# Kernel tuning notes

Hardware: AMD Instinct MI355X
Metric: run time of the kernel (lower is better)

The kernel has to match this reference:

```python
import jax, jax.numpy as jnp
import numpy as np

HEAD_DIM = 256
NUM_HEADS = 8
NUM_KV = 1
MAX_WAVELENGTH = 10000.0


def _apply_rope(x, positions):
    # x: [B, S, N, H], positions: [B, S] int
    d = x.shape[-1]
    freq_exponents = (2.0 / d) * jnp.arange(d // 2, dtype=jnp.float32)
    timescale = MAX_WAVELENGTH ** freq_exponents  # [H/2]
    radians = positions[..., None].astype(jnp.float32) / timescale  # [B, S, H/2]
    radians = radians[..., None, :]  # [B, S, 1, H/2]
    sin, cos = jnp.sin(radians), jnp.cos(radians)
    first, second = jnp.split(x.astype(jnp.float32), 2, axis=-1)
    out = jnp.concatenate([first * cos - second * sin, second * cos + first * sin], axis=-1)
    return out.astype(x.dtype)


def setup_inputs() -> dict:
    key = jax.random.key(0)
    ks = jax.random.split(key, 8)
    B, S0, S1 = 4, 768, 256
    W0, W1 = 2048, 1024
    T = S0 + S1
    s = 0.02  # param init scale
    x0 = jax.random.normal(ks[0], (B, S0, W0), jnp.float32)
    x1 = jax.random.normal(ks[1], (B, S1, W1), jnp.float32)
    w_q0 = jax.random.normal(ks[2], (NUM_HEADS, W0, HEAD_DIM), jnp.float32) * s
    w_kv0 = jax.random.normal(ks[3], (2, NUM_KV, W0, HEAD_DIM), jnp.float32) * s
    w_out0 = jax.random.normal(ks[4], (NUM_HEADS, HEAD_DIM, W0), jnp.float32) * s
    w_q1 = jax.random.normal(ks[5], (NUM_HEADS, W1, HEAD_DIM), jnp.float32) * s
    w_kv1 = jax.random.normal(ks[6], (2, NUM_KV, W1, HEAD_DIM), jnp.float32) * s
    w_out1 = jax.random.normal(ks[7], (NUM_HEADS, HEAD_DIM, W1), jnp.float32) * s
    positions = jnp.broadcast_to(jnp.arange(T, dtype=jnp.int32), (B, T))
    attn_mask = jnp.broadcast_to(jnp.tril(jnp.ones((T, T), bool))[None, None], (B, 1, T, T))
    return {"x0": x0, "x1": x1, "w_q0": w_q0, "w_kv0": w_kv0, "w_out0": w_out0,
            "w_q1": w_q1, "w_kv1": w_kv1, "w_out1": w_out1,
            "positions": positions, "attn_mask": attn_mask}


def reference(x0, x1, w_q0, w_kv0, w_out0, w_q1, w_kv1, w_out1, positions, attn_mask):
    dtype = x0.dtype
    # GQA projections per stream (num_kv_heads != num_heads path)
    q0 = jnp.einsum('BTD,NDH->BTNH', x0, w_q0)
    k0, v0 = jnp.einsum('BSD,CKDH->CBSKH', x0, w_kv0)
    q1 = jnp.einsum('BTD,NDH->BTNH', x1, w_q1)
    k1, v1 = jnp.einsum('BSD,CKDH->CBSKH', x1, w_kv1)
    q = jnp.concatenate([q0, q1], axis=1)  # [B, T, N, H]
    k = jnp.concatenate([k0, k1], axis=1)  # [B, T, K, H]
    v = jnp.concatenate([v0, v1], axis=1)
    q = _apply_rope(q, positions) * (HEAD_DIM ** -0.5)
    k = _apply_rope(k, positions)
    B, T = q.shape[0], q.shape[1]
    G = NUM_HEADS // NUM_KV
    q = q.reshape(B, T, NUM_KV, G, HEAD_DIM)
    logits = jnp.einsum('BTKGH,BSKH->BKGTS', q, k, preferred_element_type=jnp.float32)
    big_neg = -2.3819763e38
    masked = jnp.where(attn_mask[:, :, None, :, :], logits, big_neg)
    probs = jax.nn.softmax(masked, axis=-1).astype(dtype)
    encoded = jnp.einsum('BKGTS,BSKH->BTKGH', probs, v).reshape(B, T, NUM_HEADS, HEAD_DIM)
    S0 = x0.shape[1]
    out0 = jnp.einsum('BTNH,NHD->BTD', encoded[:, :S0], w_out0)
    out1 = jnp.einsum('BTNH,NHD->BTD', encoded[:, S0:], w_out1)
    return (out0, out1, k, v)
```

## Files before the change

### kernel.cpp

```cpp
#include <hip/hip_runtime.h>
#include <hip/hip_bf16.h>

typedef __attribute__((ext_vector_type(8))) short bf16x8;
typedef __attribute__((ext_vector_type(4))) float f32x4;
typedef __attribute__((ext_vector_type(4))) unsigned short u16x4;
typedef unsigned short US;

__device__ __forceinline__ f32x4 mfma16(bf16x8 a, bf16x8 b, f32x4 c) {
  return __builtin_amdgcn_mfma_f32_16x16x32_bf16(a, b, c, 0, 0, 0);
}

__device__ __forceinline__ US f2bf(float f) {
  union { float f; unsigned u; } x; x.f = f;
  unsigned r = x.u + 0x7fffu + ((x.u >> 16) & 1u);
  return (US)(r >> 16);
}

__device__ __forceinline__ void gld16(const US* gp, US* lp) {
  __builtin_amdgcn_global_load_lds(
      (const __attribute__((address_space(1))) unsigned*)gp,
      (__attribute__((address_space(3))) unsigned*)lp, 16, 0, 0);
}

__device__ __forceinline__ int map_row(int r, int mode) {
  if (mode == 1) { int b = r / 768; return b * 1024 + (r - b * 768); }
  if (mode == 2) { int b = r >> 8; return b * 1024 + 768 + (r & 255); }
  return r;
}

__global__ void k_cast(const float* __restrict__ src, US* __restrict__ dst, int n4) {
  int i = blockIdx.x * 256 + threadIdx.x;
  if (i >= n4) return;
  f32x4 v = *reinterpret_cast<const f32x4*>(src + (size_t)i * 4);
  u16x4 o;
  o[0] = f2bf(v[0]); o[1] = f2bf(v[1]); o[2] = f2bf(v[2]); o[3] = f2bf(v[3]);
  *reinterpret_cast<u16x4*>(dst + (size_t)i * 4) = o;
}

__global__ __launch_bounds__(256)
void k_tpack(const float* __restrict__ src, US* __restrict__ dst,
             int R, int C, long sbs, long dbs) {
  __shared__ float tile[32][33];
  int c0 = blockIdx.x * 32, r0 = blockIdx.y * 32;
  src += (long)blockIdx.z * sbs;
  dst += (long)blockIdx.z * dbs;
  int tx = threadIdx.x, ty = threadIdx.y;
#pragma unroll
  for (int i = 0; i < 4; ++i)
    tile[ty + 8 * i][tx] = src[(size_t)(r0 + ty + 8 * i) * C + c0 + tx];
  __syncthreads();
#pragma unroll
  for (int i = 0; i < 4; ++i)
    dst[(size_t)(c0 + ty + 8 * i) * R + r0 + tx] = f2bf(tile[tx][ty + 8 * i]);
}

template <int CMAP>
__global__ __launch_bounds__(256, 2)
void k_gemm_qkv(const US* __restrict__ A, const US* __restrict__ BT,
                float* __restrict__ Cq, float* __restrict__ Ckv,
                int M, int K) {
  __shared__ __align__(16) US lA[2][128 * 32];
  __shared__ __align__(16) US lB[2][128 * 32];
  const int tid = threadIdx.x;
  const int lane = tid & 63;
  const int wid = tid >> 6;
  const int wm = wid >> 1, wn = wid & 1;
  const int m0 = blockIdx.y * 128, n0 = blockIdx.x * 128;
  const int g = lane >> 4, c = lane & 15;
  const int lrow = lane >> 2, lcol = (lane & 3) * 8;
  const size_t ga0 = (size_t)(m0 + wid * 16 + lrow) * K + lcol;
  const size_t ga1 = (size_t)(m0 + 64 + wid * 16 + lrow) * K + lcol;
  const size_t gb0 = (size_t)(n0 + wid * 16 + lrow) * K + lcol;
  const size_t gb1 = (size_t)(n0 + 64 + wid * 16 + lrow) * K + lcol;

  auto stage = [&](int bi, int k0) {
    gld16(A + ga0 + k0, &lA[bi][(wid * 16) * 32]);
    gld16(A + ga1 + k0, &lA[bi][(64 + wid * 16) * 32]);
    gld16(BT + gb0 + k0, &lB[bi][(wid * 16) * 32]);
    gld16(BT + gb1 + k0, &lB[bi][(64 + wid * 16) * 32]);
  };

  f32x4 acc[4][4];
#pragma unroll
  for (int i = 0; i < 4; ++i)
#pragma unroll
    for (int j = 0; j < 4; ++j) acc[i][j] = f32x4{0.f, 0.f, 0.f, 0.f};

  const int nt = K >> 5;
  stage(0, 0);
  __syncthreads();
  for (int t = 0; t < nt; ++t) {
    const int bi = t & 1;
    if (t + 1 < nt) stage(bi ^ 1, (t + 1) * 32);
    bf16x8 af[4], bfr[4];
#pragma unroll
    for (int i = 0; i < 4; ++i) {
      af[i] = *reinterpret_cast<const bf16x8*>(&lA[bi][(wm * 64 + i * 16 + c) * 32 + g * 8]);
      bfr[i] = *reinterpret_cast<const bf16x8*>(&lB[bi][(wn * 64 + i * 16 + c) * 32 + g * 8]);
    }
#pragma unroll
    for (int i = 0; i < 4; ++i)
#pragma unroll
      for (int j = 0; j < 4; ++j)
        acc[i][j] = mfma16(af[i], bfr[j], acc[i][j]);
    __syncthreads();
  }

  const bool isq = (n0 < 2048);
  float* Cb = isq ? Cq : Ckv;
  const int Nst = isq ? 2048 : 512;
  const int nb = (isq ? n0 : n0 - 2048) + wn * 64 + c;
#pragma unroll
  for (int i = 0; i < 4; ++i) {
#pragma unroll
    for (int r = 0; r < 4; ++r) {
      int orow = map_row(m0 + wm * 64 + i * 16 + 4 * g + r, CMAP);
      float* cp = Cb + (size_t)orow * Nst + nb;
#pragma unroll
      for (int j = 0; j < 4; ++j) cp[j * 16] = acc[i][j][r];
    }
  }
}

__global__ __launch_bounds__(256, 2)
void k_gemm_out(const US* __restrict__ A, const US* __restrict__ BT0, const US* __restrict__ BT1,
                float* __restrict__ C0, float* __restrict__ C1) {
  const int m0 = blockIdx.y * 128, n0 = blockIdx.x * 128;
  const int s0 = m0 & 1023;
  const bool is0 = (s0 < 768);
  if (!is0 && n0 >= 1024) return;
  const US* __restrict__ BT = is0 ? BT0 : BT1;
  const int K = 2048;
  __shared__ __align__(16) US lA[2][128 * 32];
  __shared__ __align__(16) US lB[2][128 * 32];
  const int tid = threadIdx.x;
  const int lane = tid & 63;
  const int wid = tid >> 6;
  const int wm = wid >> 1, wn = wid & 1;
  const int g = lane >> 4, c = lane & 15;
  const int lrow = lane >> 2, lcol = (lane & 3) * 8;
  const size_t ga0 = (size_t)(m0 + wid * 16 + lrow) * K + lcol;
  const size_t ga1 = (size_t)(m0 + 64 + wid * 16 + lrow) * K + lcol;
  const size_t gb0 = (size_t)(n0 + wid * 16 + lrow) * K + lcol;
  const size_t gb1 = (size_t)(n0 + 64 + wid * 16 + lrow) * K + lcol;

  auto stage = [&](int bi, int k0) {
    gld16(A + ga0 + k0, &lA[bi][(wid * 16) * 32]);
    gld16(A + ga1 + k0, &lA[bi][(64 + wid * 16) * 32]);
    gld16(BT + gb0 + k0, &lB[bi][(wid * 16) * 32]);
    gld16(BT + gb1 + k0, &lB[bi][(64 + wid * 16) * 32]);
  };

  f32x4 acc[4][4];
#pragma unroll
  for (int i = 0; i < 4; ++i)
#pragma unroll
    for (int j = 0; j < 4; ++j) acc[i][j] = f32x4{0.f, 0.f, 0.f, 0.f};

  const int nt = K >> 5;
  stage(0, 0);
  __syncthreads();
  for (int t = 0; t < nt; ++t) {
    const int bi = t & 1;
    if (t + 1 < nt) stage(bi ^ 1, (t + 1) * 32);
    bf16x8 af[4], bfr[4];
#pragma unroll
    for (int i = 0; i < 4; ++i) {
      af[i] = *reinterpret_cast<const bf16x8*>(&lA[bi][(wm * 64 + i * 16 + c) * 32 + g * 8]);
      bfr[i] = *reinterpret_cast<const bf16x8*>(&lB[bi][(wn * 64 + i * 16 + c) * 32 + g * 8]);
    }
#pragma unroll
    for (int i = 0; i < 4; ++i)
#pragma unroll
      for (int j = 0; j < 4; ++j)
        acc[i][j] = mfma16(af[i], bfr[j], acc[i][j]);
    __syncthreads();
  }

  const int col = n0 + wn * 64 + c;
#pragma unroll
  for (int i = 0; i < 4; ++i) {
#pragma unroll
    for (int r = 0; r < 4; ++r) {
      const int rf = m0 + wm * 64 + i * 16 + 4 * g + r;
      const int b = rf >> 10, s = rf & 1023;
      float* cp = is0 ? (C0 + (size_t)(b * 768 + s) * 2048 + col)
                      : (C1 + (size_t)(b * 256 + s - 768) * 1024 + col);
#pragma unroll
      for (int j = 0; j < 4; ++j) cp[j * 16] = acc[i][j][r];
    }
  }
}

__global__ __launch_bounds__(256)
void k_rope(const float* __restrict__ q_raw, const float* __restrict__ kv_raw,
            const int* __restrict__ pos, US* __restrict__ q_bf,
            US* __restrict__ k_bf, float* __restrict__ k_out) {
  __shared__ float sa[128], ca[128];
  const int bt = blockIdx.x;
  const int tid = threadIdx.x;
  const int p = pos[bt];
  if (tid < 128) {
    float inv_ts = powf(10000.0f, -(float)tid * (1.0f / 128.0f));
    float r = (float)p * inv_ts;
    sa[tid] = sinf(r);
    ca[tid] = cosf(r);
  }
  __syncthreads();
  const float scale = 0.0625f;
  const size_t qo = (size_t)bt * 2048;
#pragma unroll
  for (int it = 0; it < 4; ++it) {
    int idx = it * 256 + tid;
    int n = idx >> 7, j = idx & 127;
    float x1 = q_raw[qo + n * 256 + j];
    float x2 = q_raw[qo + n * 256 + j + 128];
    float s = sa[j], co = ca[j];
    q_bf[qo + n * 256 + j] = f2bf(scale * (x1 * co - x2 * s));
    q_bf[qo + n * 256 + j + 128] = f2bf(scale * (x2 * co + x1 * s));
  }
  if (tid < 128) {
    int j = tid;
    const size_t ko = (size_t)bt * 512;
    float x1 = kv_raw[ko + j], x2 = kv_raw[ko + j + 128];
    float s = sa[j], co = ca[j];
    float o1 = x1 * co - x2 * s, o2 = x2 * co + x1 * s;
    const size_t kd = (size_t)bt * 256;
    k_bf[kd + j] = f2bf(o1);
    k_bf[kd + j + 128] = f2bf(o2);
    k_out[kd + j] = o1;
    k_out[kd + j + 128] = o2;
  }
}

__global__ __launch_bounds__(256)
void k_vtrans(const float* __restrict__ kv_raw, float* __restrict__ v_out, US* __restrict__ vt) {
  __shared__ float tile[32][33];
  int t0 = blockIdx.x * 32, h0 = blockIdx.y * 32, b = blockIdx.z;
  int tx = threadIdx.x, ty = threadIdx.y;
#pragma unroll
  for (int i = 0; i < 4; ++i) {
    int t = t0 + ty + 8 * i;
    float v = kv_raw[(size_t)(b * 1024 + t) * 512 + 256 + h0 + tx];
    tile[ty + 8 * i][tx] = v;
    v_out[(size_t)(b * 1024 + t) * 256 + h0 + tx] = v;
  }
  __syncthreads();
#pragma unroll
  for (int i = 0; i < 4; ++i) {
    int h = h0 + ty + 8 * i;
    vt[(size_t)(b * 256 + h) * 1024 + t0 + tx] = f2bf(tile[tx][ty + 8 * i]);
  }
}

__global__ __launch_bounds__(256, 2)
void k_attn(const US* __restrict__ qb, const US* __restrict__ kb,
            const US* __restrict__ vt, US* __restrict__ enc) {
  __shared__ __align__(16) US lK[2][32 * 256];
  __shared__ __align__(16) US lV[2][256 * 32];
  const int id = blockIdx.x;
  const int r0_ = (id < 256) ? id : 767 - id;
  const int qt = 63 - (r0_ >> 3);
  const int hg = (r0_ >> 2) & 1;
  const int b = r0_ & 3;
  const int tid = threadIdx.x;
  const int wid = tid >> 6;
  const int lane = tid & 63;
  const int g = lane >> 4, c = lane & 15;
  const int qbase = qt * 16;
  const int n = hg * 4 + wid;

  const US* kbB = kb + (size_t)b * 262144;
  const US* vtB = vt + (size_t)b * 262144;

  bf16x8 qf[8];
  {
    const US* qp = qb + ((size_t)((b * 1024 + qbase + c) * 8 + n)) * 256 + 8 * g;
#pragma unroll
    for (int ch = 0; ch < 8; ++ch)
      qf[ch] = *reinterpret_cast<const bf16x8*>(qp + ch * 32);
  }

  auto stage = [&](int bi, int c0) {
#pragma unroll
    for (int j = 0; j < 4; ++j) {
      const int rk = wid * 8 + j * 2 + (lane >> 5);
      const int sk = lane & 31;
      gld16(kbB + (size_t)(c0 + rk) * 256 + (sk ^ (rk & 7)) * 8,
            &lK[bi][(wid * 8 + j * 2) * 256]);
      const int rv = wid * 64 + j * 16 + (lane >> 2);
      const int sv = lane & 3;
      gld16(vtB + (size_t)rv * 1024 + c0 + (sv ^ ((rv >> 1) & 3)) * 8,
            &lV[bi][(wid * 64 + j * 16) * 32]);
    }
  };

  f32x4 acc[16];
#pragma unroll
  for (int i = 0; i < 16; ++i) acc[i] = f32x4{0.f, 0.f, 0.f, 0.f};
  float m_run = -3.0e38f, l_run = 0.f;

  const int nC = qbase / 32 + 1;
  stage(0, 0);
  __syncthreads();

  for (int i = 0; i < nC; ++i) {
    const int c0 = 32 * i;
    const int bi = i & 1;
    if (i + 1 < nC) stage(bi ^ 1, c0 + 32);

    const bool hb = (c0 + 16 <= qbase);
    f32x4 sA = {0.f, 0.f, 0.f, 0.f}, sB = {0.f, 0.f, 0.f, 0.f};
#pragma unroll
    for (int ch = 0; ch < 8; ++ch) {
      const int slot = (((ch * 4 + g) ^ (c & 7)) * 8);
      sA = mfma16(*reinterpret_cast<const bf16x8*>(&lK[bi][c * 256 + slot]), qf[ch], sA);
    }
    if (hb) {
#pragma unroll
      for (int ch = 0; ch < 8; ++ch) {
        const int slot = (((ch * 4 + g) ^ (c & 7)) * 8);
        sB = mfma16(*reinterpret_cast<const bf16x8*>(&lK[bi][(c + 16) * 256 + slot]), qf[ch], sB);
      }
    }
    if (c0 == qbase) {
#pragma unroll
      for (int r = 0; r < 4; ++r)
        if (4 * g + r > c) sA[r] = -3.0e38f;
    }
    if (hb && (c0 + 16 == qbase)) {
#pragma unroll
      for (int r = 0; r < 4; ++r)
        if (4 * g + r > c) sB[r] = -3.0e38f;
    }
    float tm = fmaxf(fmaxf(sA[0], sA[1]), fmaxf(sA[2], sA[3]));
    if (hb) tm = fmaxf(tm, fmaxf(fmaxf(sB[0], sB[1]), fmaxf(sB[2], sB[3])));
    tm = fmaxf(tm, __shfl_xor(tm, 16));
    tm = fmaxf(tm, __shfl_xor(tm, 32));
    if (!__all(tm - m_run <= 8.0f)) {
      const float m_new = fmaxf(m_run, tm);
      const float alpha = __expf(m_run - m_new);
      float aacc[4];
#pragma unroll
      for (int r = 0; r < 4; ++r) aacc[r] = __shfl(alpha, 4 * g + r);
#pragma unroll
      for (int ht = 0; ht < 16; ++ht) {
        acc[ht][0] *= aacc[0]; acc[ht][1] *= aacc[1];
        acc[ht][2] *= aacc[2]; acc[ht][3] *= aacc[3];
      }
      l_run *= alpha;
      m_run = m_new;
    }
    float pA[4], pB[4];
    float ls = 0.f;
#pragma unroll
    for (int r = 0; r < 4; ++r) { pA[r] = __expf(sA[r] - m_run); ls += pA[r]; }
#pragma unroll
    for (int r = 0; r < 4; ++r) { pB[r] = hb ? __expf(sB[r] - m_run) : 0.f; ls += pB[r]; }
    ls += __shfl_xor(ls, 16);
    ls += __shfl_xor(ls, 32);
    l_run += ls;
    bf16x8 paf;
#pragma unroll
    for (int j = 0; j < 8; ++j) {
      const int srcl = ((2 * (g & 1) + (j >> 2)) << 4) + c;
      float va = __shfl(pA[j & 3], srcl);
      float vb = __shfl(pB[j & 3], srcl);
      float pv = (g < 2) ? va : vb;
      paf[j] = (short)f2bf(pv);
    }
#pragma unroll
    for (int ht = 0; ht < 16; ++ht) {
      const int h = ht * 16 + c;
      const int slot = (g ^ ((c >> 1) & 3)) * 8;
      bf16x8 vf = *reinterpret_cast<const bf16x8*>(&lV[bi][h * 32 + slot]);
      acc[ht] = mfma16(paf, vf, acc[ht]);
    }
    __syncthreads();
  }

  const float inv = 1.0f / l_run;
  float ia[4];
#pragma unroll
  for (int r = 0; r < 4; ++r) ia[r] = __shfl(inv, 4 * g + r);
#pragma unroll
  for (int ht = 0; ht < 16; ++ht) {
#pragma unroll
    for (int r = 0; r < 4; ++r) {
      size_t o = ((size_t)((b * 1024 + qbase + 4 * g + r) * 8 + n)) * 256 + ht * 16 + c;
      enc[o] = f2bf(acc[ht][r] * ia[r]);
    }
  }
}

extern "C" void kernel_launch(void* const* d_in, const int* in_sizes, int n_in,
                              void* d_out, int out_size, void* d_ws, size_t ws_size,
                              hipStream_t stream) {
  const float* x0 = (const float*)d_in[0];
  const float* x1 = (const float*)d_in[1];
  const float* wq0 = (const float*)d_in[2];
  const float* wkv0 = (const float*)d_in[3];
  const float* wo0 = (const float*)d_in[4];
  const float* wq1 = (const float*)d_in[5];
  const float* wkv1 = (const float*)d_in[6];
  const float* wo1 = (const float*)d_in[7];
  const int* pos = (const int*)d_in[8];
  float* out = (float*)d_out;

  float* out0 = out;
  float* out1 = out + 6291456;
  float* k_out = out + 7340032;
  float* v_out = out + 8388608;

  char* ws = (char*)d_ws;
  size_t off = 0;
  auto alloc = [&](size_t bytes) {
    char* p = ws + off;
    off += (bytes + 255) & ~(size_t)255;
    return p;
  };
  US* x0b   = (US*)alloc(6291456ull * 2);
  US* x1b   = (US*)alloc(1048576ull * 2);
  US* btq0  = (US*)alloc(2048ull * 2048 * 2);
  US* btkv0 = (US*)alloc(512ull * 2048 * 2);
  US* btq1  = (US*)alloc(2048ull * 1024 * 2);
  US* btkv1 = (US*)alloc(512ull * 1024 * 2);
  US* bto0  = (US*)alloc(2048ull * 2048 * 2);
  US* bto1  = (US*)alloc(1024ull * 2048 * 2);
  float* q_raw  = (float*)alloc(8388608ull * 4);
  float* kv_raw = (float*)alloc(2097152ull * 4);
  US* q_bf = (US*)alloc(8388608ull * 2);
  US* k_bf = (US*)alloc(1048576ull * 2);
  US* vt   = (US*)alloc(1048576ull * 2 + 256);
  US* enc  = (US*)alloc(8388608ull * 2);
  (void)btkv0; (void)btkv1;

  k_cast<<<6144, 256, 0, stream>>>(x0, x0b, 1572864);
  k_cast<<<1024, 256, 0, stream>>>(x1, x1b, 262144);
  k_tpack<<<dim3(8, 64, 8), dim3(32, 8), 0, stream>>>(wq0, btq0, 2048, 256, 2048L * 256, 256L * 2048);
  k_tpack<<<dim3(8, 64, 2), dim3(32, 8), 0, stream>>>(wkv0, btkv0, 2048, 256, 2048L * 256, 256L * 2048);
  k_tpack<<<dim3(8, 32, 8), dim3(32, 8), 0, stream>>>(wq1, btq1, 1024, 256, 1024L * 256, 256L * 1024);
  k_tpack<<<dim3(8, 32, 2), dim3(32, 8), 0, stream>>>(wkv1, btkv1, 1024, 256, 1024L * 256, 256L * 1024);
  k_tpack<<<dim3(64, 64, 1), dim3(32, 8), 0, stream>>>(wo0, bto0, 2048, 2048, 0, 0);
  k_tpack<<<dim3(32, 64, 1), dim3(32, 8), 0, stream>>>(wo1, bto1, 2048, 1024, 0, 0);

  k_gemm_qkv<1><<<dim3(20, 24), 256, 0, stream>>>(x0b, btq0, q_raw, kv_raw, 3072, 2048);
  k_gemm_qkv<2><<<dim3(20, 8), 256, 0, stream>>>(x1b, btq1, q_raw, kv_raw, 1024, 1024);

  k_rope<<<4096, 256, 0, stream>>>(q_raw, kv_raw, pos, q_bf, k_bf, k_out);
  k_vtrans<<<dim3(32, 8, 4), dim3(32, 8), 0, stream>>>(kv_raw, v_out, vt);

  k_attn<<<512, 256, 0, stream>>>(q_bf, k_bf, vt, enc);

  k_gemm_out<<<dim3(16, 32), 256, 0, stream>>>(enc, bto0, bto1, out0, out1);
}
```

Baseline: 226.0 us.

## Split attention blocks to two waves, load V directly from global, split QK accumulators

```diff
diff --git a/kernel.cpp b/kernel.cpp
--- a/kernel.cpp
+++ b/kernel.cpp
@@ -253,22 +253,20 @@
   }
 }
 
-__global__ __launch_bounds__(256, 2)
+__global__ __launch_bounds__(128, 2)
 void k_attn(const US* __restrict__ qb, const US* __restrict__ kb,
             const US* __restrict__ vt, US* __restrict__ enc) {
   __shared__ __align__(16) US lK[2][32 * 256];
-  __shared__ __align__(16) US lV[2][256 * 32];
   const int id = blockIdx.x;
-  const int r0_ = (id < 256) ? id : 767 - id;
-  const int qt = 63 - (r0_ >> 3);
-  const int hg = (r0_ >> 2) & 1;
-  const int b = r0_ & 3;
+  const int qt = 63 - (id >> 4);
+  const int hg = (id >> 2) & 3;
+  const int b = id & 3;
   const int tid = threadIdx.x;
   const int wid = tid >> 6;
   const int lane = tid & 63;
   const int g = lane >> 4, c = lane & 15;
   const int qbase = qt * 16;
-  const int n = hg * 4 + wid;
+  const int n = hg * 2 + wid;
 
   const US* kbB = kb + (size_t)b * 262144;
   const US* vtB = vt + (size_t)b * 262144;
@@ -283,15 +281,12 @@
 
   auto stage = [&](int bi, int c0) {
 #pragma unroll
-    for (int j = 0; j < 4; ++j) {
-      const int rk = wid * 8 + j * 2 + (lane >> 5);
+    for (int j = 0; j < 8; ++j) {
+      const int rbase = wid * 16 + j * 2;
+      const int rk = rbase + (lane >> 5);
       const int sk = lane & 31;
       gld16(kbB + (size_t)(c0 + rk) * 256 + (sk ^ (rk & 7)) * 8,
-            &lK[bi][(wid * 8 + j * 2) * 256]);
-      const int rv = wid * 64 + j * 16 + (lane >> 2);
-      const int sv = lane & 3;
-      gld16(vtB + (size_t)rv * 1024 + c0 + (sv ^ ((rv >> 1) & 3)) * 8,
-            &lV[bi][(wid * 64 + j * 16) * 32]);
+            &lK[bi][rbase * 256]);
     }
   };
 
@@ -310,19 +305,27 @@
     if (i + 1 < nC) stage(bi ^ 1, c0 + 32);
 
     const bool hb = (c0 + 16 <= qbase);
-    f32x4 sA = {0.f, 0.f, 0.f, 0.f}, sB = {0.f, 0.f, 0.f, 0.f};
-#pragma unroll
-    for (int ch = 0; ch < 8; ++ch) {
-      const int slot = (((ch * 4 + g) ^ (c & 7)) * 8);
-      sA = mfma16(*reinterpret_cast<const bf16x8*>(&lK[bi][c * 256 + slot]), qf[ch], sA);
+    f32x4 sA0 = {0.f, 0.f, 0.f, 0.f}, sA1 = {0.f, 0.f, 0.f, 0.f};
+    f32x4 sB0 = {0.f, 0.f, 0.f, 0.f}, sB1 = {0.f, 0.f, 0.f, 0.f};
+#pragma unroll
+    for (int ch = 0; ch < 4; ++ch) {
+      const int s0_ = (((2 * ch) * 4 + g) ^ (c & 7)) * 8;
+      const int s1_ = (((2 * ch + 1) * 4 + g) ^ (c & 7)) * 8;
+      sA0 = mfma16(*reinterpret_cast<const bf16x8*>(&lK[bi][c * 256 + s0_]), qf[2 * ch], sA0);
+      sA1 = mfma16(*reinterpret_cast<const bf16x8*>(&lK[bi][c * 256 + s1_]), qf[2 * ch + 1], sA1);
     }
     if (hb) {
 #pragma unroll
-      for (int ch = 0; ch < 8; ++ch) {
-        const int slot = (((ch * 4 + g) ^ (c & 7)) * 8);
-        sB = mfma16(*reinterpret_cast<const bf16x8*>(&lK[bi][(c + 16) * 256 + slot]), qf[ch], sB);
+      for (int ch = 0; ch < 4; ++ch) {
+        const int s0_ = (((2 * ch) * 4 + g) ^ (c & 7)) * 8;
+        const int s1_ = (((2 * ch + 1) * 4 + g) ^ (c & 7)) * 8;
+        sB0 = mfma16(*reinterpret_cast<const bf16x8*>(&lK[bi][(c + 16) * 256 + s0_]), qf[2 * ch], sB0);
+        sB1 = mfma16(*reinterpret_cast<const bf16x8*>(&lK[bi][(c + 16) * 256 + s1_]), qf[2 * ch + 1], sB1);
       }
     }
+    f32x4 sA, sB;
+#pragma unroll
+    for (int r = 0; r < 4; ++r) { sA[r] = sA0[r] + sA1[r]; sB[r] = sB0[r] + sB1[r]; }
     if (c0 == qbase) {
 #pragma unroll
       for (int r = 0; r < 4; ++r)
@@ -369,11 +372,10 @@
       float pv = (g < 2) ? va : vb;
       paf[j] = (short)f2bf(pv);
     }
+    const US* vb2 = vtB + c0 + (size_t)c * 1024 + 8 * g;
 #pragma unroll
     for (int ht = 0; ht < 16; ++ht) {
-      const int h = ht * 16 + c;
-      const int slot = (g ^ ((c >> 1) & 3)) * 8;
-      bf16x8 vf = *reinterpret_cast<const bf16x8*>(&lV[bi][h * 32 + slot]);
+      bf16x8 vf = *reinterpret_cast<const bf16x8*>(vb2 + (size_t)ht * 16384);
       acc[ht] = mfma16(paf, vf, acc[ht]);
     }
     __syncthreads();
@@ -450,7 +452,7 @@
   k_rope<<<4096, 256, 0, stream>>>(q_raw, kv_raw, pos, q_bf, k_bf, k_out);
   k_vtrans<<<dim3(32, 8, 4), dim3(32, 8), 0, stream>>>(kv_raw, v_out, vt);
 
-  k_attn<<<512, 256, 0, stream>>>(q_bf, k_bf, vt, enc);
+  k_attn<<<1024, 128, 0, stream>>>(q_bf, k_bf, vt, enc);
 
   k_gemm_out<<<dim3(16, 32), 256, 0, stream>>>(enc, bto0, bto1, out0, out1);
 }
```

Result: slower. 264.8 us (+17.1%).

## Fuse Q RoPE into QKV GEMM epilogue, merge prep launches, precompute sincos

Applied to the files above, without the earlier changes.

```diff
diff --git a/kernel.cpp b/kernel.cpp
--- a/kernel.cpp
+++ b/kernel.cpp
@@ -22,43 +22,80 @@
       (__attribute__((address_space(3))) unsigned*)lp, 16, 0, 0);
 }
 
+__device__ __forceinline__ int permq(int h) {
+  return ((h >> 5) << 6) + (h & 15) + (((h >> 4) & 1) << 5);
+}
+
 __device__ __forceinline__ int map_row(int r, int mode) {
   if (mode == 1) { int b = r / 768; return b * 1024 + (r - b * 768); }
   if (mode == 2) { int b = r >> 8; return b * 1024 + 768 + (r & 255); }
   return r;
 }
 
-__global__ void k_cast(const float* __restrict__ src, US* __restrict__ dst, int n4) {
-  int i = blockIdx.x * 256 + threadIdx.x;
-  if (i >= n4) return;
-  f32x4 v = *reinterpret_cast<const f32x4*>(src + (size_t)i * 4);
-  u16x4 o;
-  o[0] = f2bf(v[0]); o[1] = f2bf(v[1]); o[2] = f2bf(v[2]); o[3] = f2bf(v[3]);
-  *reinterpret_cast<u16x4*>(dst + (size_t)i * 4) = o;
-}
-
 __global__ __launch_bounds__(256)
-void k_tpack(const float* __restrict__ src, US* __restrict__ dst,
-             int R, int C, long sbs, long dbs) {
+void k_sincos(const int* __restrict__ pos, float2* __restrict__ sct) {
+  int idx = blockIdx.x * 256 + threadIdx.x;
+  int bt = idx >> 7, j = idx & 127;
+  float inv_ts = powf(10000.0f, -(float)j * (1.0f / 128.0f));
+  float r = (float)pos[bt] * inv_ts;
+  sct[idx] = make_float2(sinf(r), cosf(r));
+}
+
+__global__ __launch_bounds__(256)
+void k_prep(const float* __restrict__ x0, const float* __restrict__ x1,
+            US* __restrict__ x0b, US* __restrict__ x1b,
+            const float* __restrict__ wq0, const float* __restrict__ wkv0,
+            const float* __restrict__ wq1, const float* __restrict__ wkv1,
+            const float* __restrict__ wo0, const float* __restrict__ wo1,
+            US* __restrict__ btq0, US* __restrict__ btkv0,
+            US* __restrict__ btq1, US* __restrict__ btkv1,
+            US* __restrict__ bto0, US* __restrict__ bto1) {
+  const int bid = blockIdx.x;
+  const int tid = threadIdx.x;
+  if (bid < 7168) {
+    const float* src; US* dst; int i;
+    if (bid < 6144) { src = x0; dst = x0b; i = bid * 256 + tid; }
+    else            { src = x1; dst = x1b; i = (bid - 6144) * 256 + tid; }
+    f32x4 v = *reinterpret_cast<const f32x4*>(src + (size_t)i * 4);
+    u16x4 o;
+    o[0] = f2bf(v[0]); o[1] = f2bf(v[1]); o[2] = f2bf(v[2]); o[3] = f2bf(v[3]);
+    *reinterpret_cast<u16x4*>(dst + (size_t)i * 4) = o;
+    return;
+  }
   __shared__ float tile[32][33];
-  int c0 = blockIdx.x * 32, r0 = blockIdx.y * 32;
-  src += (long)blockIdx.z * sbs;
-  dst += (long)blockIdx.z * dbs;
-  int tx = threadIdx.x, ty = threadIdx.y;
+  const float* src; US* dst; int R, C, CX, local; long sbs, dbs; bool pq = false;
+  if (bid < 11264)      { local = bid - 7168;  src = wq0;  dst = btq0;  R = 2048; C = 256;  CX = 8;  sbs = 2048L * 256; dbs = 256L * 2048; pq = true; }
+  else if (bid < 12288) { local = bid - 11264; src = wkv0; dst = btkv0; R = 2048; C = 256;  CX = 8;  sbs = 2048L * 256; dbs = 256L * 2048; }
+  else if (bid < 14336) { local = bid - 12288; src = wq1;  dst = btq1;  R = 1024; C = 256;  CX = 8;  sbs = 1024L * 256; dbs = 256L * 1024; pq = true; }
+  else if (bid < 14848) { local = bid - 14336; src = wkv1; dst = btkv1; R = 1024; C = 256;  CX = 8;  sbs = 1024L * 256; dbs = 256L * 1024; }
+  else if (bid < 18944) { local = bid - 14848; src = wo0;  dst = bto0;  R = 2048; C = 2048; CX = 64; sbs = 0; dbs = 0; }
+  else                  { local = bid - 18944; src = wo1;  dst = bto1;  R = 2048; C = 1024; CX = 32; sbs = 0; dbs = 0; }
+  const int RY = R >> 5;
+  const int cx = local % CX;
+  const int rest = local / CX;
+  const int ry = rest % RY;
+  const int z = rest / RY;
+  const int c0 = cx * 32, r0 = ry * 32;
+  const int tx = tid & 31, ty = tid >> 5;
+  src += (long)z * sbs;
+  dst += (long)z * dbs;
 #pragma unroll
   for (int i = 0; i < 4; ++i)
     tile[ty + 8 * i][tx] = src[(size_t)(r0 + ty + 8 * i) * C + c0 + tx];
   __syncthreads();
 #pragma unroll
-  for (int i = 0; i < 4; ++i)
-    dst[(size_t)(c0 + ty + 8 * i) * R + r0 + tx] = f2bf(tile[tx][ty + 8 * i]);
+  for (int i = 0; i < 4; ++i) {
+    int h = c0 + ty + 8 * i;
+    int ph = pq ? ((h < 128) ? permq(h) : permq(h - 128) + 16) : h;
+    dst[(size_t)ph * R + r0 + tx] = f2bf(tile[tx][ty + 8 * i]);
+  }
 }
 
 template <int CMAP>
 __global__ __launch_bounds__(256, 2)
 void k_gemm_qkv(const US* __restrict__ A, const US* __restrict__ BT,
-                float* __restrict__ Cq, float* __restrict__ Ckv,
-                int M, int K) {
+                US* __restrict__ q_bf, float* __restrict__ Ckv,
+                const float2* __restrict__ sct, int M, int K) {
   __shared__ __align__(16) US lA[2][128 * 32];
   __shared__ __align__(16) US lB[2][128 * 32];
   const int tid = threadIdx.x;
@@ -106,18 +143,39 @@
     __syncthreads();
   }
 
-  const bool isq = (n0 < 2048);
-  float* Cb = isq ? Cq : Ckv;
-  const int Nst = isq ? 2048 : 512;
-  const int nb = (isq ? n0 : n0 - 2048) + wn * 64 + c;
-#pragma unroll
-  for (int i = 0; i < 4; ++i) {
-#pragma unroll
-    for (int r = 0; r < 4; ++r) {
-      int orow = map_row(m0 + wm * 64 + i * 16 + 4 * g + r, CMAP);
-      float* cp = Cb + (size_t)orow * Nst + nb;
-#pragma unroll
-      for (int j = 0; j < 4; ++j) cp[j * 16] = acc[i][j][r];
+  const int colb = n0 + wn * 64;
+  if (colb < 2048) {
+    const int n = colb >> 8;
+    const int base64 = colb & 255;
+    const int h0 = (base64 >> 6) * 32 + c;
+    const float scale = 0.0625f;
+#pragma unroll
+    for (int i = 0; i < 4; ++i) {
+#pragma unroll
+      for (int r = 0; r < 4; ++r) {
+        const int orow = map_row(m0 + wm * 64 + i * 16 + 4 * g + r, CMAP);
+        const float2 sc0 = sct[orow * 128 + h0];
+        const float2 sc1 = sct[orow * 128 + h0 + 16];
+        US* qp = q_bf + ((size_t)orow * 8 + n) * 256 + base64 + c;
+        const float q1 = acc[i][0][r], q2 = acc[i][1][r];
+        const float q3 = acc[i][2][r], q4 = acc[i][3][r];
+        qp[0]  = f2bf(scale * (q1 * sc0.y - q2 * sc0.x));
+        qp[16] = f2bf(scale * (q2 * sc0.y + q1 * sc0.x));
+        qp[32] = f2bf(scale * (q3 * sc1.y - q4 * sc1.x));
+        qp[48] = f2bf(scale * (q4 * sc1.y + q3 * sc1.x));
+      }
+    }
+  } else {
+    const int nb = colb - 2048 + c;
+#pragma unroll
+    for (int i = 0; i < 4; ++i) {
+#pragma unroll
+      for (int r = 0; r < 4; ++r) {
+        const int orow = map_row(m0 + wm * 64 + i * 16 + 4 * g + r, CMAP);
+        float* cp = Ckv + (size_t)orow * 512 + nb;
+#pragma unroll
+        for (int j = 0; j < 4; ++j) cp[j * 16] = acc[i][j][r];
+      }
     }
   }
 }
@@ -192,45 +250,21 @@
   }
 }
 
-__global__ __launch_bounds__(256)
-void k_rope(const float* __restrict__ q_raw, const float* __restrict__ kv_raw,
-            const int* __restrict__ pos, US* __restrict__ q_bf,
-            US* __restrict__ k_bf, float* __restrict__ k_out) {
-  __shared__ float sa[128], ca[128];
+__global__ __launch_bounds__(128)
+void k_ropek(const float* __restrict__ kv_raw, const float2* __restrict__ sct,
+             US* __restrict__ k_bf, float* __restrict__ k_out) {
   const int bt = blockIdx.x;
-  const int tid = threadIdx.x;
-  const int p = pos[bt];
-  if (tid < 128) {
-    float inv_ts = powf(10000.0f, -(float)tid * (1.0f / 128.0f));
-    float r = (float)p * inv_ts;
-    sa[tid] = sinf(r);
-    ca[tid] = cosf(r);
-  }
-  __syncthreads();
-  const float scale = 0.0625f;
-  const size_t qo = (size_t)bt * 2048;
-#pragma unroll
-  for (int it = 0; it < 4; ++it) {
-    int idx = it * 256 + tid;
-    int n = idx >> 7, j = idx & 127;
-    float x1 = q_raw[qo + n * 256 + j];
-    float x2 = q_raw[qo + n * 256 + j + 128];
-    float s = sa[j], co = ca[j];
-    q_bf[qo + n * 256 + j] = f2bf(scale * (x1 * co - x2 * s));
-    q_bf[qo + n * 256 + j + 128] = f2bf(scale * (x2 * co + x1 * s));
-  }
-  if (tid < 128) {
-    int j = tid;
-    const size_t ko = (size_t)bt * 512;
-    float x1 = kv_raw[ko + j], x2 = kv_raw[ko + j + 128];
-    float s = sa[j], co = ca[j];
-    float o1 = x1 * co - x2 * s, o2 = x2 * co + x1 * s;
-    const size_t kd = (size_t)bt * 256;
-    k_bf[kd + j] = f2bf(o1);
-    k_bf[kd + j + 128] = f2bf(o2);
-    k_out[kd + j] = o1;
-    k_out[kd + j + 128] = o2;
-  }
+  const int j = threadIdx.x;
+  const size_t ko = (size_t)bt * 512;
+  const float x1 = kv_raw[ko + j], x2 = kv_raw[ko + j + 128];
+  const float2 sc = sct[bt * 128 + j];
+  const float o1 = x1 * sc.y - x2 * sc.x, o2 = x2 * sc.y + x1 * sc.x;
+  const size_t kd = (size_t)bt * 256;
+  const int p = permq(j);
+  k_bf[kd + p] = f2bf(o1);
+  k_bf[kd + p + 16] = f2bf(o2);
+  k_out[kd + j] = o1;
+  k_out[kd + j + 128] = o2;
 }
 
 __global__ __launch_bounds__(256)
@@ -311,6 +345,7 @@
 
     const bool hb = (c0 + 16 <= qbase);
     f32x4 sA = {0.f, 0.f, 0.f, 0.f}, sB = {0.f, 0.f, 0.f, 0.f};
+    __builtin_amdgcn_s_setprio(1);
 #pragma unroll
     for (int ch = 0; ch < 8; ++ch) {
       const int slot = (((ch * 4 + g) ^ (c & 7)) * 8);
@@ -323,6 +358,7 @@
         sB = mfma16(*reinterpret_cast<const bf16x8*>(&lK[bi][(c + 16) * 256 + slot]), qf[ch], sB);
       }
     }
+    __builtin_amdgcn_s_setprio(0);
     if (c0 == qbase) {
 #pragma unroll
       for (int r = 0; r < 4; ++r)
@@ -369,6 +405,7 @@
       float pv = (g < 2) ? va : vb;
       paf[j] = (short)f2bf(pv);
     }
+    __builtin_amdgcn_s_setprio(1);
 #pragma unroll
     for (int ht = 0; ht < 16; ++ht) {
       const int h = ht * 16 + c;
@@ -376,6 +413,7 @@
       bf16x8 vf = *reinterpret_cast<const bf16x8*>(&lV[bi][h * 32 + slot]);
       acc[ht] = mfma16(paf, vf, acc[ht]);
     }
+    __builtin_amdgcn_s_setprio(0);
     __syncthreads();
   }
 
@@ -427,27 +465,22 @@
   US* btkv1 = (US*)alloc(512ull * 1024 * 2);
   US* bto0  = (US*)alloc(2048ull * 2048 * 2);
   US* bto1  = (US*)alloc(1024ull * 2048 * 2);
-  float* q_raw  = (float*)alloc(8388608ull * 4);
   float* kv_raw = (float*)alloc(2097152ull * 4);
   US* q_bf = (US*)alloc(8388608ull * 2);
   US* k_bf = (US*)alloc(1048576ull * 2);
   US* vt   = (US*)alloc(1048576ull * 2 + 256);
   US* enc  = (US*)alloc(8388608ull * 2);
-  (void)btkv0; (void)btkv1;
-
-  k_cast<<<6144, 256, 0, stream>>>(x0, x0b, 1572864);
-  k_cast<<<1024, 256, 0, stream>>>(x1, x1b, 262144);
-  k_tpack<<<dim3(8, 64, 8), dim3(32, 8), 0, stream>>>(wq0, btq0, 2048, 256, 2048L * 256, 256L * 2048);
-  k_tpack<<<dim3(8, 64, 2), dim3(32, 8), 0, stream>>>(wkv0, btkv0, 2048, 256, 2048L * 256, 256L * 2048);
-  k_tpack<<<dim3(8, 32, 8), dim3(32, 8), 0, stream>>>(wq1, btq1, 1024, 256, 1024L * 256, 256L * 1024);
-  k_tpack<<<dim3(8, 32, 2), dim3(32, 8), 0, stream>>>(wkv1, btkv1, 1024, 256, 1024L * 256, 256L * 1024);
-  k_tpack<<<dim3(64, 64, 1), dim3(32, 8), 0, stream>>>(wo0, bto0, 2048, 2048, 0, 0);
-  k_tpack<<<dim3(32, 64, 1), dim3(32, 8), 0, stream>>>(wo1, bto1, 2048, 1024, 0, 0);
-
-  k_gemm_qkv<1><<<dim3(20, 24), 256, 0, stream>>>(x0b, btq0, q_raw, kv_raw, 3072, 2048);
-  k_gemm_qkv<2><<<dim3(20, 8), 256, 0, stream>>>(x1b, btq1, q_raw, kv_raw, 1024, 1024);
-
-  k_rope<<<4096, 256, 0, stream>>>(q_raw, kv_raw, pos, q_bf, k_bf, k_out);
+  float2* sct = (float2*)alloc(524288ull * 8);
+
+  k_sincos<<<2048, 256, 0, stream>>>(pos, sct);
+
+  k_prep<<<20992, 256, 0, stream>>>(x0, x1, x0b, x1b, wq0, wkv0, wq1, wkv1, wo0, wo1,
+                                    btq0, btkv0, btq1, btkv1, bto0, bto1);
+
+  k_gemm_qkv<1><<<dim3(20, 24), 256, 0, stream>>>(x0b, btq0, q_bf, kv_raw, sct, 3072, 2048);
+  k_gemm_qkv<2><<<dim3(20, 8), 256, 0, stream>>>(x1b, btq1, q_bf, kv_raw, sct, 1024, 1024);
+
+  k_ropek<<<4096, 128, 0, stream>>>(kv_raw, sct, k_bf, k_out);
   k_vtrans<<<dim3(32, 8, 4), dim3(32, 8), 0, stream>>>(kv_raw, v_out, vt);
 
   k_attn<<<512, 256, 0, stream>>>(q_bf, k_bf, vt, enc);
```

New measurement: 215.4 us. -4.7%, faster.
